# Kernel tuning notes

Hardware: AMD Instinct MI355X
Metric: run time of the kernel (lower is better)

## Reference

```python
import jax, jax.numpy as jnp
import numpy as np

BLOCK = 32          # Q4_0 block size
Q_ZERO = 8.0        # 4-bit zero point


def setup_inputs() -> dict:
    key = jax.random.key(0)
    k1, k2, k3, k4 = jax.random.split(key, 4)
    O, I = 8192, 8192
    nb = I // BLOCK                      # 256 blocks per row
    x = jax.random.normal(k1, (4096, I), dtype=jnp.float32)
    # packed Q4_0 payload: 16 bytes per block, each byte holds two 4-bit quants
    qweight = jax.random.randint(k2, (O, nb, BLOCK // 2), 0, 256, dtype=jnp.int32)
    scales = jax.random.uniform(k3, (O, nb), dtype=jnp.float32)
    bias = jax.random.normal(k4, (O,), dtype=jnp.float32)
    return {"x": x, "qweight": qweight, "scales": scales, "bias": bias}


def _dequantize_q4_0(qweight, scales):
    # qweight: [O, NB, 16] bytes; low nibble -> elems 0..15, high nibble -> 16..31
    O, nb, _ = qweight.shape
    low = qweight & 0xF
    high = (qweight >> 4) & 0xF
    vals = jnp.concatenate([low, high], axis=-1).astype(scales.dtype)  # [O, NB, 32]
    w = (vals - Q_ZERO) * scales[..., None]                            # [O, NB, 32]
    return w.reshape(O, nb * BLOCK)                                    # [O, I]


def reference(x, qweight, scales, bias):
    # GGUFLayer.cast_bias_weight: dequantize weight/bias to input dtype, then linear
    w = _dequantize_q4_0(qweight, scales).astype(x.dtype)  # [O, I]
    b = bias.astype(x.dtype)
    return jnp.einsum('ni,oi->no', x, w) + b               # F.linear(x, w, b)
```

## Files before the change

### kernel.cpp

```cpp
#include <hip/hip_runtime.h>
#include <stdint.h>

#define M_DIM 4096
#define N_DIM 8192
#define K_DIM 8192
#define NB    256

#define BM 256
#define BN 256
#define BK 64

typedef __attribute__((ext_vector_type(8)))  __bf16 bf16x8;
typedef __attribute__((ext_vector_type(16))) float  floatx16;
typedef __attribute__((ext_vector_type(4)))  unsigned short ushort4v;
typedef __attribute__((ext_vector_type(8)))  unsigned short ushort8;

__device__ __forceinline__ unsigned short f32_to_bf16_rne(float f) {
    union { float f; unsigned int u; } v; v.f = f;
    unsigned int u = v.u;
    u += 0x7FFFu + ((u >> 16) & 1u);
    return (unsigned short)(u >> 16);
}

__global__ __launch_bounds__(256) void dequant_w(const int* __restrict__ q,
                                                 const float* __restrict__ sc,
                                                 unsigned short* __restrict__ w) {
    const int tid = blockIdx.x * 256 + threadIdx.x;
    int4 v = ((const int4*)q)[tid];
    const int blk = tid >> 2;
    const int s   = tid & 3;
    const float scale = sc[blk];
    int by[4] = { v.x, v.y, v.z, v.w };
    ushort4v lo, hi;
#pragma unroll
    for (int j = 0; j < 4; ++j) {
        lo[j] = f32_to_bf16_rne((float)((by[j] & 0xF) - 8) * scale);
        hi[j] = f32_to_bf16_rne((float)(((by[j] >> 4) & 0xF) - 8) * scale);
    }
    unsigned short* base = w + (size_t)blk * 32 + s * 4;
    *(ushort4v*)(base)      = lo;
    *(ushort4v*)(base + 16) = hi;
}

__global__ __launch_bounds__(256) void convert_x(const float* __restrict__ x,
                                                 unsigned short* __restrict__ xb) {
    size_t idx = ((size_t)blockIdx.x * 256 + threadIdx.x) * 8;
    float4 f0 = *(const float4*)(x + idx);
    float4 f1 = *(const float4*)(x + idx + 4);
    ushort8 o;
    o[0] = f32_to_bf16_rne(f0.x); o[1] = f32_to_bf16_rne(f0.y);
    o[2] = f32_to_bf16_rne(f0.z); o[3] = f32_to_bf16_rne(f0.w);
    o[4] = f32_to_bf16_rne(f1.x); o[5] = f32_to_bf16_rne(f1.y);
    o[6] = f32_to_bf16_rne(f1.z); o[7] = f32_to_bf16_rne(f1.w);
    *(ushort8*)(xb + idx) = o;
}

__device__ __forceinline__ void load_lds16(const unsigned short* g, unsigned short* l) {
    __builtin_amdgcn_global_load_lds(
        (const __attribute__((address_space(1))) unsigned int*)(g),
        (__attribute__((address_space(3))) unsigned int*)(l),
        16, 0, 0);
}

__device__ __forceinline__ floatx16 mfma_op(bf16x8 a, bf16x8 b, floatx16 c) {
    return __builtin_amdgcn_mfma_f32_32x32x16_bf16(a, b, c, 0, 0, 0);
}

#define SL(kk, F) (((((kk) * 2) + q5) ^ (F)) * 8)

#define STAGE_A(b, h, kb) do { \
    load_lds16(gA + (size_t)((h) * 128 +  0) * K_DIM + (kb) * BK, &lsA[b][((h) * 128 +  0 + wave * 8) * BK]); \
    load_lds16(gA + (size_t)((h) * 128 + 64) * K_DIM + (kb) * BK, &lsA[b][((h) * 128 + 64 + wave * 8) * BK]); \
} while (0)
#define STAGE_B(b, h, kb) do { \
    load_lds16(gB + (size_t)((h) * 128 +  0) * K_DIM + (kb) * BK, &lsB[b][((h) * 128 +  0 + wave * 8) * BK]); \
    load_lds16(gB + (size_t)((h) * 128 + 64) * K_DIM + (kb) * BK, &lsB[b][((h) * 128 + 64 + wave * 8) * BK]); \
} while (0)

#define PH_HEAD __builtin_amdgcn_s_barrier(); \
                asm volatile("s_waitcnt lgkmcnt(0)" ::: "memory"); \
                __builtin_amdgcn_s_setprio(1)
#define PH_TAIL __builtin_amdgcn_s_setprio(0)

#define TILE(bb, S1, S2, S3, S4, VMW) do { \
     \
    _Pragma("unroll") for (int kk = 0; kk < 4; ++kk) { \
        aL[0][kk] = *(const bf16x8*)(&lsA[bb][aA0 + SL(kk, F0)]); \
        aL[1][kk] = *(const bf16x8*)(&lsA[bb][aA1 + SL(kk, F1)]); \
        b0[kk]    = *(const bf16x8*)(&lsB[bb][aB0 + SL(kk, F0)]); \
    } \
    S1; PH_HEAD; \
    _Pragma("unroll") for (int kk = 0; kk < 4; ++kk) { \
        acc[0][0] = mfma_op(aL[0][kk], b0[kk], acc[0][0]); \
        acc[1][0] = mfma_op(aL[1][kk], b0[kk], acc[1][0]); \
    } \
    PH_TAIL; __builtin_amdgcn_s_barrier(); \
     \
    _Pragma("unroll") for (int kk = 0; kk < 4; ++kk) \
        b1[kk] = *(const bf16x8*)(&lsB[bb][aB1 + SL(kk, F1)]); \
    S2; PH_HEAD; \
    _Pragma("unroll") for (int kk = 0; kk < 4; ++kk) { \
        acc[0][1] = mfma_op(aL[0][kk], b1[kk], acc[0][1]); \
        acc[1][1] = mfma_op(aL[1][kk], b1[kk], acc[1][1]); \
    } \
    PH_TAIL; __builtin_amdgcn_s_barrier(); \
     \
    _Pragma("unroll") for (int kk = 0; kk < 4; ++kk) { \
        aH[0][kk] = *(const bf16x8*)(&lsA[bb][aA2 + SL(kk, F0)]); \
        aH[1][kk] = *(const bf16x8*)(&lsA[bb][aA3 + SL(kk, F1)]); \
    } \
    S3; PH_HEAD; \
    _Pragma("unroll") for (int kk = 0; kk < 4; ++kk) { \
        acc[2][0] = mfma_op(aH[0][kk], b0[kk], acc[2][0]); \
        acc[3][0] = mfma_op(aH[1][kk], b0[kk], acc[3][0]); \
    } \
    PH_TAIL; __builtin_amdgcn_s_barrier(); \
     \
    S4; __builtin_amdgcn_s_barrier(); __builtin_amdgcn_s_setprio(1); \
    _Pragma("unroll") for (int kk = 0; kk < 4; ++kk) { \
        acc[2][1] = mfma_op(aH[0][kk], b1[kk], acc[2][1]); \
        acc[3][1] = mfma_op(aH[1][kk], b1[kk], acc[3][1]); \
    } \
    __builtin_amdgcn_s_setprio(0); VMW; __builtin_amdgcn_s_barrier(); \
} while (0)

__global__ __launch_bounds__(512, 2) void gemm_bt(const unsigned short* __restrict__ A,
                                                  const unsigned short* __restrict__ B,
                                                  const float* __restrict__ bias,
                                                  float* __restrict__ C) {
    __shared__ unsigned short lsA[2][BM * BK];
    __shared__ unsigned short lsB[2][BN * BK];

    const int tid  = threadIdx.x;
    const int wave = tid >> 6;
    const int lane = tid & 63;
    const int wm = wave >> 2;
    const int wn = wave & 3;

    const int bid = blockIdx.x;
    const int wg  = (bid & 7) * 64 + (bid >> 3);
    const int m0 = (wg >> 5) * BM;
    const int n0 = (wg & 31) * BN;

    const int lrow = lane >> 3;
    const int l7s  = lane & 7;
    const int csrc = ((l7s ^ lrow ^ wave) & 7) * 8;
    const unsigned short* gA = A + (size_t)(m0 + wave * 8 + lrow) * K_DIM + csrc;
    const unsigned short* gB = B + (size_t)(n0 + wave * 8 + lrow) * K_DIM + csrc;

    const int q5  = lane >> 5;
    const int r31 = lane & 31;
    const int l7  = lane & 7;
    const int rh  = r31 >> 3;
    const int aA0 = (wm * 128 +  0 + r31) * BK;
    const int aA1 = (wm * 128 + 32 + r31) * BK;
    const int aA2 = (wm * 128 + 64 + r31) * BK;
    const int aA3 = (wm * 128 + 96 + r31) * BK;
    const int aB0 = (wn * 64  +  0 + r31) * BK;
    const int aB1 = (wn * 64  + 32 + r31) * BK;
    const int F0  = l7 ^ (rh & 7);
    const int F1  = l7 ^ ((4 + rh) & 7);

    floatx16 acc[4][2] = {};
    bf16x8 aL[2][4], aH[2][4], b0[4], b1[4];

    STAGE_B(0, 0, 0); STAGE_B(0, 1, 0);
    STAGE_A(0, 0, 0); STAGE_A(0, 1, 0);
    STAGE_B(1, 0, 1); STAGE_B(1, 1, 1);
    asm volatile("s_waitcnt vmcnt(4)" ::: "memory");
    __builtin_amdgcn_s_barrier();

    for (int i = 0; i < 63; ++i) {
        const int t0 = 2 * i;
        TILE(0, STAGE_A(1, 0, t0 + 1), STAGE_A(1, 1, t0 + 1),
                STAGE_B(0, 0, t0 + 2), STAGE_B(0, 1, t0 + 2),
                asm volatile("s_waitcnt vmcnt(4)" ::: "memory"));
        TILE(1, STAGE_A(0, 0, t0 + 2), STAGE_A(0, 1, t0 + 2),
                STAGE_B(1, 0, t0 + 3), STAGE_B(1, 1, t0 + 3),
                asm volatile("s_waitcnt vmcnt(4)" ::: "memory"));
    }
    TILE(0, STAGE_A(1, 0, 127), STAGE_A(1, 1, 127), (void)0, (void)0,
            asm volatile("s_waitcnt vmcnt(0)" ::: "memory"));
    TILE(1, (void)0, (void)0, (void)0, (void)0, (void)0);

#pragma unroll
    for (int fj = 0; fj < 2; ++fj) {
        const int col = n0 + wn * 64 + fj * 32 + r31;
        const float bv = bias[col];
#pragma unroll
        for (int fi = 0; fi < 4; ++fi) {
            const int rowbase = m0 + wm * 128 + fi * 32 + q5 * 4;
#pragma unroll
            for (int r = 0; r < 16; ++r) {
                const int row = rowbase + (r & 3) + 8 * (r >> 2);
                C[(size_t)row * N_DIM + col] = acc[fi][fj][r] + bv;
            }
        }
    }
}

extern "C" void kernel_launch(void* const* d_in, const int* in_sizes, int n_in,
                              void* d_out, int out_size, void* d_ws, size_t ws_size,
                              hipStream_t stream) {
    (void)in_sizes; (void)n_in; (void)out_size; (void)ws_size;
    const float* x    = (const float*)d_in[0];
    const int*   qw   = (const int*)d_in[1];
    const float* sc   = (const float*)d_in[2];
    const float* bias = (const float*)d_in[3];
    float* out = (float*)d_out;

    unsigned short* Wb = (unsigned short*)d_ws;
    unsigned short* Xb = (unsigned short*)((char*)d_ws + (size_t)N_DIM * K_DIM * 2);

    dequant_w<<<dim3((N_DIM * NB * 4) / 256), dim3(256), 0, stream>>>(qw, sc, Wb);
    convert_x<<<dim3((size_t)M_DIM * K_DIM / (256 * 8)), dim3(256), 0, stream>>>(x, Xb);
    gemm_bt<<<dim3((M_DIM / BM) * (N_DIM / BN)), dim3(512), 0, stream>>>(Xb, Wb, bias, out);
}
```

Before: 801.9 us.

## Restructure GEMM tile phases, remap block swizzle, and rework dequant/convert kernels

The GEMM inner tile is reorganized so that each phase loads one A fragment set and computes it against both B fragments. The next A fragment's LDS reads are issued before the current MFMA phase, with sched_barriers and a reduced set of waits. The workgroup-to-tile mapping changes so that each XCD-interleaved group covers two adjacent M rows across all N tiles, aiming for better L2 reuse. The dequant kernel now writes contiguous 8-element bf16 vectors per thread by reading two int4 words, and convert_x handles 4 floats per thread instead of 8. The tile restructure raises VGPR pressure, since four A fragments and both B fragments are live at once, which risks occupancy under the 2-waves-per-SIMD bound.

```diff
diff --git a/kernel.cpp b/kernel.cpp
--- a/kernel.cpp
+++ b/kernel.cpp
@@ -22,37 +22,33 @@
     return (unsigned short)(u >> 16);
 }
 
-__global__ __launch_bounds__(256) void dequant_w(const int* __restrict__ q,
+__global__ __launch_bounds__(256) void dequant_w(const int* __restrict__ qw,
                                                  const float* __restrict__ sc,
                                                  unsigned short* __restrict__ w) {
     const int tid = blockIdx.x * 256 + threadIdx.x;
-    int4 v = ((const int4*)q)[tid];
     const int blk = tid >> 2;
-    const int s   = tid & 3;
+    const int q   = tid & 3;
+    const int4* src = (const int4*)qw + (size_t)blk * 4 + (q & 1) * 2;
+    int4 v0 = src[0];
+    int4 v1 = src[1];
     const float scale = sc[blk];
-    int by[4] = { v.x, v.y, v.z, v.w };
-    ushort4v lo, hi;
-#pragma unroll
-    for (int j = 0; j < 4; ++j) {
-        lo[j] = f32_to_bf16_rne((float)((by[j] & 0xF) - 8) * scale);
-        hi[j] = f32_to_bf16_rne((float)(((by[j] >> 4) & 0xF) - 8) * scale);
-    }
-    unsigned short* base = w + (size_t)blk * 32 + s * 4;
-    *(ushort4v*)(base)      = lo;
-    *(ushort4v*)(base + 16) = hi;
+    const int sh = (q >> 1) * 4;
+    int by[8] = { v0.x, v0.y, v0.z, v0.w, v1.x, v1.y, v1.z, v1.w };
+    ushort8 o;
+#pragma unroll
+    for (int j = 0; j < 8; ++j)
+        o[j] = f32_to_bf16_rne((float)(((by[j] >> sh) & 0xF) - 8) * scale);
+    *(ushort8*)(w + (size_t)blk * 32 + q * 8) = o;
 }
 
 __global__ __launch_bounds__(256) void convert_x(const float* __restrict__ x,
                                                  unsigned short* __restrict__ xb) {
-    size_t idx = ((size_t)blockIdx.x * 256 + threadIdx.x) * 8;
-    float4 f0 = *(const float4*)(x + idx);
-    float4 f1 = *(const float4*)(x + idx + 4);
-    ushort8 o;
-    o[0] = f32_to_bf16_rne(f0.x); o[1] = f32_to_bf16_rne(f0.y);
-    o[2] = f32_to_bf16_rne(f0.z); o[3] = f32_to_bf16_rne(f0.w);
-    o[4] = f32_to_bf16_rne(f1.x); o[5] = f32_to_bf16_rne(f1.y);
-    o[6] = f32_to_bf16_rne(f1.z); o[7] = f32_to_bf16_rne(f1.w);
-    *(ushort8*)(xb + idx) = o;
+    size_t idx = ((size_t)blockIdx.x * 256 + threadIdx.x) * 4;
+    float4 f = *(const float4*)(x + idx);
+    ushort4v o;
+    o[0] = f32_to_bf16_rne(f.x); o[1] = f32_to_bf16_rne(f.y);
+    o[2] = f32_to_bf16_rne(f.z); o[3] = f32_to_bf16_rne(f.w);
+    *(ushort4v*)(xb + idx) = o;
 }
 
 __device__ __forceinline__ void load_lds16(const unsigned short* g, unsigned short* l) {
@@ -77,51 +73,41 @@
     load_lds16(gB + (size_t)((h) * 128 + 64) * K_DIM + (kb) * BK, &lsB[b][((h) * 128 + 64 + wave * 8) * BK]); \
 } while (0)
 
-#define PH_HEAD __builtin_amdgcn_s_barrier(); \
-                asm volatile("s_waitcnt lgkmcnt(0)" ::: "memory"); \
-                __builtin_amdgcn_s_setprio(1)
-#define PH_TAIL __builtin_amdgcn_s_setprio(0)
+#define RD4(dst, ls, OFF, F) \
+    _Pragma("unroll") for (int kk = 0; kk < 4; ++kk) \
+        dst[kk] = *(const bf16x8*)(&(ls)[(OFF) + SL(kk, F)]);
+
+#define CL(ai, av) \
+    _Pragma("unroll") for (int kk = 0; kk < 4; ++kk) { \
+        acc[ai][0] = mfma_op(av[kk], b0[kk], acc[ai][0]); \
+        acc[ai][1] = mfma_op(av[kk], b1[kk], acc[ai][1]); \
+    }
+
+#define PH_WAIT asm volatile("s_waitcnt lgkmcnt(0)" ::: "memory"); \
+                __builtin_amdgcn_sched_barrier(0)
+#define SB0     __builtin_amdgcn_sched_barrier(0)
+#define PRIO1   __builtin_amdgcn_s_setprio(1)
+#define PRIO0   __builtin_amdgcn_s_setprio(0)
+#define BAR     __builtin_amdgcn_s_barrier()
 
 #define TILE(bb, S1, S2, S3, S4, VMW) do { \
      \
-    _Pragma("unroll") for (int kk = 0; kk < 4; ++kk) { \
-        aL[0][kk] = *(const bf16x8*)(&lsA[bb][aA0 + SL(kk, F0)]); \
-        aL[1][kk] = *(const bf16x8*)(&lsA[bb][aA1 + SL(kk, F1)]); \
-        b0[kk]    = *(const bf16x8*)(&lsB[bb][aB0 + SL(kk, F0)]); \
-    } \
-    S1; PH_HEAD; \
-    _Pragma("unroll") for (int kk = 0; kk < 4; ++kk) { \
-        acc[0][0] = mfma_op(aL[0][kk], b0[kk], acc[0][0]); \
-        acc[1][0] = mfma_op(aL[1][kk], b0[kk], acc[1][0]); \
-    } \
-    PH_TAIL; __builtin_amdgcn_s_barrier(); \
-     \
-    _Pragma("unroll") for (int kk = 0; kk < 4; ++kk) \
-        b1[kk] = *(const bf16x8*)(&lsB[bb][aB1 + SL(kk, F1)]); \
-    S2; PH_HEAD; \
-    _Pragma("unroll") for (int kk = 0; kk < 4; ++kk) { \
-        acc[0][1] = mfma_op(aL[0][kk], b1[kk], acc[0][1]); \
-        acc[1][1] = mfma_op(aL[1][kk], b1[kk], acc[1][1]); \
-    } \
-    PH_TAIL; __builtin_amdgcn_s_barrier(); \
-     \
-    _Pragma("unroll") for (int kk = 0; kk < 4; ++kk) { \
-        aH[0][kk] = *(const bf16x8*)(&lsA[bb][aA2 + SL(kk, F0)]); \
-        aH[1][kk] = *(const bf16x8*)(&lsA[bb][aA3 + SL(kk, F1)]); \
-    } \
-    S3; PH_HEAD; \
-    _Pragma("unroll") for (int kk = 0; kk < 4; ++kk) { \
-        acc[2][0] = mfma_op(aH[0][kk], b0[kk], acc[2][0]); \
-        acc[3][0] = mfma_op(aH[1][kk], b0[kk], acc[3][0]); \
-    } \
-    PH_TAIL; __builtin_amdgcn_s_barrier(); \
-     \
-    S4; __builtin_amdgcn_s_barrier(); __builtin_amdgcn_s_setprio(1); \
-    _Pragma("unroll") for (int kk = 0; kk < 4; ++kk) { \
-        acc[2][1] = mfma_op(aH[0][kk], b1[kk], acc[2][1]); \
-        acc[3][1] = mfma_op(aH[1][kk], b1[kk], acc[3][1]); \
-    } \
-    __builtin_amdgcn_s_setprio(0); VMW; __builtin_amdgcn_s_barrier(); \
+    RD4(b0, lsB[bb], aB0, F0); RD4(b1, lsB[bb], aB1, F1); RD4(a0, lsA[bb], aA0, F0); \
+    S1; BAR; PH_WAIT; \
+    RD4(a1, lsA[bb], aA1, F1); SB0; \
+    PRIO1; CL(0, a0); PRIO0; BAR; \
+     \
+    S2; BAR; PH_WAIT; \
+    RD4(a2, lsA[bb], aA2, F0); SB0; \
+    PRIO1; CL(1, a1); PRIO0; BAR; \
+     \
+    S3; BAR; PH_WAIT; \
+    RD4(a3, lsA[bb], aA3, F1); SB0; \
+    PRIO1; CL(2, a2); PRIO0; BAR; \
+     \
+    S4; BAR; PH_WAIT; \
+    PRIO1; CL(3, a3); PRIO0; \
+    VMW; BAR; \
 } while (0)
 
 __global__ __launch_bounds__(512, 2) void gemm_bt(const unsigned short* __restrict__ A,
@@ -138,9 +124,10 @@
     const int wn = wave & 3;
 
     const int bid = blockIdx.x;
-    const int wg  = (bid & 7) * 64 + (bid >> 3);
-    const int m0 = (wg >> 5) * BM;
-    const int n0 = (wg & 31) * BN;
+    const int x8  = bid & 7;
+    const int j   = bid >> 3;
+    const int m0 = (x8 * 2 + (j >> 5)) * BM;
+    const int n0 = (j & 31) * BN;
 
     const int lrow = lane >> 3;
     const int l7s  = lane & 7;
@@ -162,13 +149,13 @@
     const int F1  = l7 ^ ((4 + rh) & 7);
 
     floatx16 acc[4][2] = {};
-    bf16x8 aL[2][4], aH[2][4], b0[4], b1[4];
+    bf16x8 a0[4], a1[4], a2[4], a3[4], b0[4], b1[4];
 
     STAGE_B(0, 0, 0); STAGE_B(0, 1, 0);
     STAGE_A(0, 0, 0); STAGE_A(0, 1, 0);
     STAGE_B(1, 0, 1); STAGE_B(1, 1, 1);
     asm volatile("s_waitcnt vmcnt(4)" ::: "memory");
-    __builtin_amdgcn_s_barrier();
+    BAR;
 
     for (int i = 0; i < 63; ++i) {
         const int t0 = 2 * i;
@@ -190,10 +177,11 @@
 #pragma unroll
         for (int fi = 0; fi < 4; ++fi) {
             const int rowbase = m0 + wm * 128 + fi * 32 + q5 * 4;
+            const floatx16 av = acc[fi][fj];
 #pragma unroll
             for (int r = 0; r < 16; ++r) {
                 const int row = rowbase + (r & 3) + 8 * (r >> 2);
-                C[(size_t)row * N_DIM + col] = acc[fi][fj][r] + bv;
+                C[(size_t)row * N_DIM + col] = av[r] + bv;
             }
         }
     }
@@ -213,6 +201,6 @@
     unsigned short* Xb = (unsigned short*)((char*)d_ws + (size_t)N_DIM * K_DIM * 2);
 
     dequant_w<<<dim3((N_DIM * NB * 4) / 256), dim3(256), 0, stream>>>(qw, sc, Wb);
-    convert_x<<<dim3((size_t)M_DIM * K_DIM / (256 * 8)), dim3(256), 0, stream>>>(x, Xb);
+    convert_x<<<dim3((size_t)M_DIM * K_DIM / (256 * 4)), dim3(256), 0, stream>>>(x, Xb);
     gemm_bt<<<dim3((M_DIM / BM) * (N_DIM / BN)), dim3(512), 0, stream>>>(Xb, Wb, bias, out);
 }
```

Measured after the change: 859.5 us. 7.2% more time.
